# Kernel optimization log

Measured on AMD Instinct MI355X. Metric: run time of the kernel, lower is better.

## Reference

```python
import jax, jax.numpy as jnp
import numpy as np

B, S, E, H, R = 512, 50, 128, 8, 32
D = E // H  # depth per head
USERS, ITEMS, ALLSEQ, NCLASS = 50000, 20000, 20000, 5


def setup_inputs() -> dict:
    key = jax.random.key(0)
    ks = jax.random.split(key, 20)
    n = lambda k, shp, s=0.05: jax.random.normal(k, shp, dtype=jnp.float32) * s
    return {
        "user": jax.random.randint(ks[0], (B,), 0, USERS),
        "item": jax.random.randint(ks[1], (B,), 0, ITEMS),
        "neighbor": jax.random.randint(ks[2], (B, S), 0, USERS),
        "seq": jax.random.randint(ks[3], (B, S), 0, ALLSEQ),
        "user_emb_table": n(ks[4], (USERS, E)),
        "item_emb_table": n(ks[5], (ITEMS, E)),
        "user_item_LCU": n(ks[6], (ALLSEQ, R, E), 0.01),
        "item_user_LCU": n(ks[7], (ALLSEQ, R, E), 0.01),
        "wq": n(ks[8], (E, E)), "bq": jnp.zeros((E,), jnp.float32),
        "wk": n(ks[9], (E, E)), "bk": jnp.zeros((E,), jnp.float32),
        "wv": n(ks[10], (E, E)), "bv": jnp.zeros((E,), jnp.float32),
        "wo": n(ks[11], (E, E)), "bo": jnp.zeros((E,), jnp.float32),
        "fc_w": n(ks[12], (R, NCLASS)), "fc_b": jnp.zeros((NCLASS,), jnp.float32),
    }


def _forward(user, item, neighbor, seq,
             user_emb_table, item_emb_table, user_item_LCU, item_user_LCU,
             wq, bq, wk, bk, wv, bv, wo, bo, fc_w, fc_b):
    user_emb = user_emb_table[user]            # [B,E]
    neighbor_emb = user_emb_table[neighbor]    # [B,S,E]
    item_emb = item_emb_table[item]            # [B,E]
    weight = (neighbor > 0).astype(jnp.float32)  # [B,S] padding mask (1=real)

    # ---- single-query multi-head attention (use_attention=True) ----
    q = (user_emb @ wq + bq).reshape(B, H, D)                       # [B,H,D]
    k = (neighbor_emb @ wk + bk).reshape(B, S, H, D).transpose(0, 2, 1, 3)  # [B,H,S,D]
    v = (neighbor_emb @ wv + bv).reshape(B, S, H, D).transpose(0, 2, 1, 3)  # [B,H,S,D]
    logits = jnp.einsum('bhd,bhsd->bhs', q, k) / jnp.sqrt(jnp.float32(D))
    logits = logits + (1.0 - weight)[:, None, :] * (-1e9)           # mask padding
    attn = jax.nn.softmax(logits, axis=-1)                          # [B,H,S]
    ctx = attn[..., None] * v                                       # [B,H,S,D]
    ctx = ctx.transpose(0, 2, 1, 3).reshape(B, S, E)                # [B,S,E]
    neighbor_emb = ctx @ wo + bo                                    # [B,S,E]

    # ---- region embedding ----
    K_ui = user_item_LCU[seq]   # [B,S,R,E]
    K_iu = item_user_LCU[seq]   # [B,S,R,E]
    neighbor_profile = jnp.einsum('bsre,bse->bsr', K_iu, neighbor_emb)  # [B,S,R]
    item_profile = jnp.einsum('bsre,be->bsr', K_ui, item_emb)          # [B,S,R]
    neighbor_rating = neighbor_profile * item_profile * weight[:, :, None]
    user_rating_vector = jnp.max(neighbor_rating, axis=1)              # [B,R]

    # ---- rating classifier ----
    return jax.nn.softmax(user_rating_vector @ fc_w + fc_b, axis=-1)   # [B,NCLASS]


def reference(user, item, neighbor, seq,
              user_emb_table, item_emb_table, user_item_LCU, item_user_LCU,
              wq, bq, wk, bk, wv, bv, wo, bo, fc_w, fc_b):
    return _forward(user, item, neighbor, seq,
                    user_emb_table, item_emb_table, user_item_LCU, item_user_LCU,
                    wq, bq, wk, bk, wv, bv, wo, bo, fc_w, fc_b)
```

## Files before the change

### kernel.cpp

```cpp
#include <hip/hip_runtime.h>
#include <math.h>

#define BB 512
#define SS 50
#define EE 128
#define HH 8
#define RR 32
#define NC 5
#define NSEQ 20000
#define NBS (BB*SS)
#define LDK 136

typedef __attribute__((ext_vector_type(8))) __bf16 bf16x8;
typedef __attribute__((ext_vector_type(4))) float f32x4;
typedef __attribute__((ext_vector_type(4))) unsigned short us4;

__device__ __forceinline__ unsigned short f2bf(float f) {
    unsigned int u = __float_as_uint(f);
    unsigned int r = (u + 0x7fffu + ((u >> 16) & 1u)) >> 16;
    return (unsigned short)r;
}
__device__ __forceinline__ float bf2f(unsigned short s) {
    return __uint_as_float(((unsigned int)s) << 16);
}
__device__ __forceinline__ float dot4(const float4& a, const float4& b) {
    return a.x*b.x + a.y*b.y + a.z*b.z + a.w*b.w;
}

__global__ __launch_bounds__(128) void conv_kernel(const float* __restrict__ wv,
                                                   const float* __restrict__ wo,
                                                   unsigned short* __restrict__ wvT,
                                                   unsigned short* __restrict__ woT) {
    const int n = blockIdx.x & 127;
    const float* src = (blockIdx.x >> 7) ? wo : wv;
    unsigned short* dst = (blockIdx.x >> 7) ? woT : wvT;
    const int k = threadIdx.x;
    dst[n*EE + k] = f2bf(src[k*EE + n]);
}

__global__ __launch_bounds__(256) void hist_kernel(const int* __restrict__ seq,
                                                   int* __restrict__ hist) {
    int i = blockIdx.x * 256 + threadIdx.x;
    if (i < NBS) atomicAdd(&hist[seq[i]], 1);
}

__global__ __launch_bounds__(1024) void scan_kernel(int* __restrict__ hist,
                                                    int* __restrict__ hstart) {
    const int t = threadIdx.x;
    const int CH = 20;
    const int base = t * CH;
    int loc[CH];
    int s = 0;
    #pragma unroll
    for (int i = 0; i < CH; ++i) {
        int idx = base + i;
        int v = (idx < NSEQ) ? hist[idx] : 0;
        loc[i] = s; s += v;
    }
    const int lane = t & 63, w = t >> 6;
    int incl = s;
    #pragma unroll
    for (int off = 1; off < 64; off <<= 1) {
        int n = __shfl_up(incl, off);
        if (lane >= off) incl += n;
    }
    __shared__ int wsum[16];
    if (lane == 63) wsum[w] = incl;
    __syncthreads();
    if (t == 0) {
        int acc = 0;
        #pragma unroll
        for (int k = 0; k < 16; ++k) { int v = wsum[k]; wsum[k] = acc; acc += v; }
    }
    __syncthreads();
    const int excl = incl - s + wsum[w];
    #pragma unroll
    for (int i = 0; i < CH; ++i) {
        int idx = base + i;
        if (idx < NSEQ) {
            int e = excl + loc[i];
            hist[idx] = e;
            hstart[idx] = e;
        }
    }
    if (t == 0) hstart[NSEQ] = NBS;
}

__global__ __launch_bounds__(256) void scatter_kernel(const int* __restrict__ seq,
                                                      int* __restrict__ hist,
                                                      int* __restrict__ perm) {
    int i = blockIdx.x * 256 + threadIdx.x;
    if (i < NBS) {
        int pos = atomicAdd(&hist[seq[i]], 1);
        perm[pos] = i;
    }
}

__global__ __launch_bounds__(256, 4) void attn_kernel(
    const int* __restrict__ user,
    const int* __restrict__ neighbor,
    const float* __restrict__ uet,
    const float* __restrict__ wq, const float* __restrict__ bq,
    const float* __restrict__ wk, const float* __restrict__ bk,
    const float* __restrict__ bv, const float* __restrict__ bo,
    const unsigned short* __restrict__ wvT, const unsigned short* __restrict__ woT,
    float* __restrict__ ws_ne2)
{
    __shared__ unsigned short kA[64*LDK];
    __shared__ float ue[EE];
    __shared__ float qs[EE];
    __shared__ float qkv[EE][HH];
    __shared__ float qkb[HH];
    __shared__ float attn_s[HH][SS];
    __shared__ float maskadd[SS];

    const int b = blockIdx.x;
    const int t = threadIdx.x;

    if (t < EE) ue[t] = uet[(size_t)user[b]*EE + t];
    if (t < SS) maskadd[t] = (neighbor[b*SS + t] > 0) ? 0.f : -1e9f;
    for (int idx = t; idx < SS*32; idx += 256) {
        int s = idx >> 5, g = idx & 31;
        float4 v = ((const float4*)(uet + (size_t)neighbor[b*SS + s]*EE))[g];
        us4 o; o.x = f2bf(v.x); o.y = f2bf(v.y); o.z = f2bf(v.z); o.w = f2bf(v.w);
        *(us4*)&kA[s*LDK + g*4] = o;
    }
    for (int idx = t; idx < 14*LDK; idx += 256) {
        kA[50*LDK + idx] = 0;
    }
    __syncthreads();

    if (t < EE) {
        float acc = bq[t];
        #pragma unroll 4
        for (int e = 0; e < EE; ++e) acc = fmaf(ue[e], wq[e*EE + t], acc);
        qs[t] = acc;
    }
    __syncthreads();

    {
        const int e = t >> 1, h0 = (t & 1) * 4;
        const float* wrow = wk + e*EE;
        #pragma unroll
        for (int j = 0; j < 4; ++j) {
            int h = h0 + j;
            float acc = 0.f;
            #pragma unroll
            for (int d = 0; d < 16; ++d) acc = fmaf(qs[h*16 + d], wrow[h*16 + d], acc);
            qkv[e][h] = acc;
        }
    }
    if (t < HH) {
        float acc = 0.f;
        #pragma unroll
        for (int d = 0; d < 16; ++d) acc = fmaf(qs[t*16 + d], bk[t*16 + d], acc);
        qkb[t] = acc;
    }
    __syncthreads();

    if (t < HH*SS) {
        const int s = t >> 3, h = t & 7;
        float acc = 0.f;
        for (int e = 0; e < EE; ++e) {
            acc = fmaf(bf2f(kA[s*LDK + e]), qkv[e][h], acc);
        }
        attn_s[h][s] = (acc + qkb[h]) * 0.25f + maskadd[s];
    }
    __syncthreads();

    if (t < 64) {
        int h = t >> 3, l = t & 7;
        float mx = -3e38f;
        #pragma unroll
        for (int i = 0; i < 7; ++i) { int s = i*8 + l; if (s < SS) mx = fmaxf(mx, attn_s[h][s]); }
        mx = fmaxf(mx, __shfl_xor(mx, 1));
        mx = fmaxf(mx, __shfl_xor(mx, 2));
        mx = fmaxf(mx, __shfl_xor(mx, 4));
        float ev[7]; float sm_ = 0.f;
        #pragma unroll
        for (int i = 0; i < 7; ++i) {
            int s = i*8 + l; ev[i] = 0.f;
            if (s < SS) { ev[i] = expf(attn_s[h][s] - mx); sm_ += ev[i]; }
        }
        sm_ += __shfl_xor(sm_, 1);
        sm_ += __shfl_xor(sm_, 2);
        sm_ += __shfl_xor(sm_, 4);
        float inv = 1.f / sm_;
        #pragma unroll
        for (int i = 0; i < 7; ++i) { int s = i*8 + l; if (s < SS) attn_s[h][s] = ev[i] * inv; }
    }
    __syncthreads();

    const int w    = t >> 6;
    const int l    = t & 63;
    const int lrow = l & 15;
    const int kg   = l >> 4;

    bf16x8 a0 = *(const bf16x8*)&kA[(w*16 + lrow)*LDK +  0 + kg*8];
    bf16x8 a1 = *(const bf16x8*)&kA[(w*16 + lrow)*LDK + 32 + kg*8];
    bf16x8 a2 = *(const bf16x8*)&kA[(w*16 + lrow)*LDK + 64 + kg*8];
    bf16x8 a3 = *(const bf16x8*)&kA[(w*16 + lrow)*LDK + 96 + kg*8];

    f32x4 acc[8];
    #pragma unroll
    for (int nt = 0; nt < 8; ++nt) {
        const unsigned short* bp = wvT + (nt*16 + lrow)*EE + kg*8;
        bf16x8 b0 = *(const bf16x8*)&bp[0];
        bf16x8 b1 = *(const bf16x8*)&bp[32];
        bf16x8 b2 = *(const bf16x8*)&bp[64];
        bf16x8 b3 = *(const bf16x8*)&bp[96];
        f32x4 c = {0.f, 0.f, 0.f, 0.f};
        c = __builtin_amdgcn_mfma_f32_16x16x32_bf16(a0, b0, c, 0, 0, 0);
        c = __builtin_amdgcn_mfma_f32_16x16x32_bf16(a1, b1, c, 0, 0, 0);
        c = __builtin_amdgcn_mfma_f32_16x16x32_bf16(a2, b2, c, 0, 0, 0);
        c = __builtin_amdgcn_mfma_f32_16x16x32_bf16(a3, b3, c, 0, 0, 0);
        acc[nt] = c;
    }

    #pragma unroll
    for (int nt = 0; nt < 8; ++nt) {
        const int col = nt*16 + lrow;
        const float bvc = bv[col];
        #pragma unroll
        for (int rg = 0; rg < 4; ++rg) {
            const int row = w*16 + kg*4 + rg;
            const float av = (row < SS) ? attn_s[nt][row] : 0.f;
            kA[row*LDK + col] = f2bf((acc[nt][rg] + bvc) * av);
        }
    }
    __syncthreads();

    bf16x8 c0 = *(const bf16x8*)&kA[(w*16 + lrow)*LDK +  0 + kg*8];
    bf16x8 c1 = *(const bf16x8*)&kA[(w*16 + lrow)*LDK + 32 + kg*8];
    bf16x8 c2 = *(const bf16x8*)&kA[(w*16 + lrow)*LDK + 64 + kg*8];
    bf16x8 c3 = *(const bf16x8*)&kA[(w*16 + lrow)*LDK + 96 + kg*8];

    #pragma unroll
    for (int nt = 0; nt < 8; ++nt) {
        const unsigned short* bp = woT + (nt*16 + lrow)*EE + kg*8;
        bf16x8 b0 = *(const bf16x8*)&bp[0];
        bf16x8 b1 = *(const bf16x8*)&bp[32];
        bf16x8 b2 = *(const bf16x8*)&bp[64];
        bf16x8 b3 = *(const bf16x8*)&bp[96];
        f32x4 c = {0.f, 0.f, 0.f, 0.f};
        c = __builtin_amdgcn_mfma_f32_16x16x32_bf16(c0, b0, c, 0, 0, 0);
        c = __builtin_amdgcn_mfma_f32_16x16x32_bf16(c1, b1, c, 0, 0, 0);
        c = __builtin_amdgcn_mfma_f32_16x16x32_bf16(c2, b2, c, 0, 0, 0);
        c = __builtin_amdgcn_mfma_f32_16x16x32_bf16(c3, b3, c, 0, 0, 0);
        const int col = nt*16 + lrow;
        const float boc = bo[col];
        #pragma unroll
        for (int rg = 0; rg < 4; ++rg) {
            const int row = w*16 + kg*4 + rg;
            if (row < SS)
                ws_ne2[((size_t)b*SS + row)*EE + col] = c[rg] + boc;
        }
    }
}

__global__ __launch_bounds__(256, 6) void region_kernel(
    const int* __restrict__ neighbor, const int* __restrict__ item,
    const float* __restrict__ ui_lcu, const float* __restrict__ iu_lcu,
    const float* __restrict__ iet, const float* __restrict__ ws_ne2,
    const int* __restrict__ hstart, const int* __restrict__ perm,
    float* __restrict__ ws_rating)
{
    const int j = blockIdx.x;
    const int start = hstart[j];
    const int end   = hstart[j + 1];
    if (start >= end) return;

    const int t = threadIdx.x;
    const int r = t >> 3, l = t & 7;

    const float4* kiu_g = (const float4*)(iu_lcu + ((size_t)j*RR + r)*EE);
    const float4* kui_g = (const float4*)(ui_lcu + ((size_t)j*RR + r)*EE);
    float4 kiu_r[4], kui_r[4];
    #pragma unroll
    for (int i = 0; i < 4; ++i) {
        int c = l + 8*i;
        kiu_r[i] = kiu_g[c];
        kui_r[i] = kui_g[c];
    }

    __shared__ float ner[EE], ier[EE];
    const float4* n4 = (const float4*)ner;
    const float4* i4 = (const float4*)ier;

    for (int o = start; o < end; ++o) {
        const int bs = perm[o];
        const int b  = bs / SS;
        if (t < EE) ner[t] = ws_ne2[(size_t)bs*EE + t];
        else        ier[t - EE] = iet[(size_t)item[b]*EE + (t - EE)];
        __syncthreads();

        float np_ = 0.f, ip_ = 0.f;
        #pragma unroll
        for (int i = 0; i < 4; ++i) {
            int c = l + 8*i;
            np_ += dot4(kiu_r[i], n4[c]);
            ip_ += dot4(kui_r[i], i4[c]);
        }
        np_ += __shfl_xor(np_, 1); np_ += __shfl_xor(np_, 2); np_ += __shfl_xor(np_, 4);
        ip_ += __shfl_xor(ip_, 1); ip_ += __shfl_xor(ip_, 2); ip_ += __shfl_xor(ip_, 4);

        const float w = (neighbor[bs] > 0) ? 1.f : 0.f;
        if (l == 0) ws_rating[(size_t)bs*RR + r] = np_ * ip_ * w;
        if (o + 1 < end) __syncthreads();
    }
}

__global__ __launch_bounds__(256) void head_kernel(
    const float* __restrict__ ws_rating,
    const float* __restrict__ fc_w, const float* __restrict__ fc_b,
    float* __restrict__ out)
{
    __shared__ float part[8][RR];
    __shared__ float urv[RR];
    __shared__ float lg[NC];
    const int b = blockIdx.x, t = threadIdx.x;
    const int r = t & 31, sub = t >> 5;

    float m = -3e38f;
    for (int s = sub; s < SS; s += 8)
        m = fmaxf(m, ws_rating[((size_t)b*SS + s)*RR + r]);
    part[sub][r] = m;
    __syncthreads();
    if (t < RR) {
        float mm = part[0][t];
        #pragma unroll
        for (int k = 1; k < 8; ++k) mm = fmaxf(mm, part[k][t]);
        urv[t] = mm;
    }
    __syncthreads();
    if (t < NC) {
        float acc = fc_b[t];
        #pragma unroll
        for (int rr = 0; rr < RR; ++rr) acc = fmaf(urv[rr], fc_w[rr*NC + t], acc);
        lg[t] = acc;
    }
    __syncthreads();
    if (t < NC) {
        float mx = lg[0];
        #pragma unroll
        for (int c = 1; c < NC; ++c) mx = fmaxf(mx, lg[c]);
        float sm = 0.f;
        #pragma unroll
        for (int c = 0; c < NC; ++c) sm += expf(lg[c] - mx);
        out[b*NC + t] = expf(lg[t] - mx) / sm;
    }
}

extern "C" void kernel_launch(void* const* d_in, const int* in_sizes, int n_in,
                              void* d_out, int out_size, void* d_ws, size_t ws_size,
                              hipStream_t stream) {
    const int*   user     = (const int*)d_in[0];
    const int*   item     = (const int*)d_in[1];
    const int*   neighbor = (const int*)d_in[2];
    const int*   seq      = (const int*)d_in[3];
    const float* uet      = (const float*)d_in[4];
    const float* iet      = (const float*)d_in[5];
    const float* ui_lcu   = (const float*)d_in[6];
    const float* iu_lcu   = (const float*)d_in[7];
    const float* wq = (const float*)d_in[8];   const float* bq = (const float*)d_in[9];
    const float* wk = (const float*)d_in[10];  const float* bk = (const float*)d_in[11];
    const float* wv = (const float*)d_in[12];  const float* bv = (const float*)d_in[13];
    const float* wo = (const float*)d_in[14];  const float* bo = (const float*)d_in[15];
    const float* fcw = (const float*)d_in[16]; const float* fcb = (const float*)d_in[17];

    float* ws = (float*)d_ws;
    float* ws_ne2    = ws;
    float* ws_rating = ws_ne2 + (size_t)BB*SS*EE;
    unsigned short* wvT = (unsigned short*)(ws_rating + (size_t)BB*SS*RR);
    unsigned short* woT = wvT + EE*EE;
    int*   hist      = (int*)(woT + EE*EE);
    int*   hstart    = hist + NSEQ;
    int*   perm      = hstart + NSEQ + 1;
    float* out = (float*)d_out;

    hipLaunchKernelGGL(conv_kernel, dim3(256), dim3(128), 0, stream, wv, wo, wvT, woT);
    hipMemsetAsync(hist, 0, NSEQ * sizeof(int), stream);
    hipLaunchKernelGGL(hist_kernel, dim3((NBS + 255)/256), dim3(256), 0, stream, seq, hist);
    hipLaunchKernelGGL(scan_kernel, dim3(1), dim3(1024), 0, stream, hist, hstart);
    hipLaunchKernelGGL(scatter_kernel, dim3((NBS + 255)/256), dim3(256), 0, stream, seq, hist, perm);

    hipLaunchKernelGGL(attn_kernel, dim3(BB), dim3(256), 0, stream,
                       user, neighbor, uet,
                       wq, bq, wk, bk, bv, bo, wvT, woT, ws_ne2);

    hipLaunchKernelGGL(region_kernel, dim3(NSEQ), dim3(256), 0, stream,
                       neighbor, item, ui_lcu, iu_lcu, iet, ws_ne2, hstart, perm, ws_rating);

    hipLaunchKernelGGL(head_kernel, dim3(BB), dim3(256), 0, stream,
                       ws_rating, fcw, fcb, out);
}
```

Baseline: 182.9 us.

## Compute attention logits with MFMA and drop shared staging in region kernel

The attention kernel now stores the folded q·Wk vectors as a bf16 transposed tile and computes the 50×8 logits with 16x16x32 bf16 MFMA, reusing the neighbor A-fragments later for the V projection. This replaces a serial 128-step scalar FMA loop per thread. The region kernel now reads neighbor and item embeddings directly from global memory instead of staging them in shared memory, which removes two barriers per iteration, and it loads the LCU rows with nontemporal loads. The costs are bf16 rounding of the q·Wk product and redundant global reads across the 32 r-groups, which mostly hit cache.

```diff
diff --git a/kernel.cpp b/kernel.cpp
--- a/kernel.cpp
+++ b/kernel.cpp
@@ -20,11 +20,11 @@
     unsigned int r = (u + 0x7fffu + ((u >> 16) & 1u)) >> 16;
     return (unsigned short)r;
 }
-__device__ __forceinline__ float bf2f(unsigned short s) {
-    return __uint_as_float(((unsigned int)s) << 16);
-}
 __device__ __forceinline__ float dot4(const float4& a, const float4& b) {
     return a.x*b.x + a.y*b.y + a.z*b.z + a.w*b.w;
+}
+__device__ __forceinline__ float dot4v(const f32x4& a, const float4& b) {
+    return a[0]*b.x + a[1]*b.y + a[2]*b.z + a[3]*b.w;
 }
 
 __global__ __launch_bounds__(128) void conv_kernel(const float* __restrict__ wv,
@@ -107,27 +107,26 @@
     float* __restrict__ ws_ne2)
 {
     __shared__ unsigned short kA[64*LDK];
+    __shared__ unsigned short qkvT[16][EE];
     __shared__ float ue[EE];
     __shared__ float qs[EE];
-    __shared__ float qkv[EE][HH];
     __shared__ float qkb[HH];
-    __shared__ float attn_s[HH][SS];
-    __shared__ float maskadd[SS];
+    __shared__ float attn_s[HH][64];
+    __shared__ float maskadd[64];
 
     const int b = blockIdx.x;
     const int t = threadIdx.x;
 
     if (t < EE) ue[t] = uet[(size_t)user[b]*EE + t];
-    if (t < SS) maskadd[t] = (neighbor[b*SS + t] > 0) ? 0.f : -1e9f;
+    if (t < 64) maskadd[t] = (t < SS && neighbor[b*SS + t] > 0) ? 0.f : -1e9f;
     for (int idx = t; idx < SS*32; idx += 256) {
         int s = idx >> 5, g = idx & 31;
         float4 v = ((const float4*)(uet + (size_t)neighbor[b*SS + s]*EE))[g];
         us4 o; o.x = f2bf(v.x); o.y = f2bf(v.y); o.z = f2bf(v.z); o.w = f2bf(v.w);
         *(us4*)&kA[s*LDK + g*4] = o;
     }
-    for (int idx = t; idx < 14*LDK; idx += 256) {
-        kA[50*LDK + idx] = 0;
-    }
+    for (int idx = t; idx < 14*LDK; idx += 256) kA[50*LDK + idx] = 0;
+    for (int idx = t; idx < 8*EE; idx += 256) qkvT[8 + (idx >> 7)][idx & 127] = 0;
     __syncthreads();
 
     if (t < EE) {
@@ -147,7 +146,7 @@
             float acc = 0.f;
             #pragma unroll
             for (int d = 0; d < 16; ++d) acc = fmaf(qs[h*16 + d], wrow[h*16 + d], acc);
-            qkv[e][h] = acc;
+            qkvT[h][e] = f2bf(acc);
         }
     }
     if (t < HH) {
@@ -158,28 +157,49 @@
     }
     __syncthreads();
 
-    if (t < HH*SS) {
-        const int s = t >> 3, h = t & 7;
-        float acc = 0.f;
-        for (int e = 0; e < EE; ++e) {
-            acc = fmaf(bf2f(kA[s*LDK + e]), qkv[e][h], acc);
-        }
-        attn_s[h][s] = (acc + qkb[h]) * 0.25f + maskadd[s];
+    const int w    = t >> 6;
+    const int l    = t & 63;
+    const int lrow = l & 15;
+    const int kg   = l >> 4;
+
+    bf16x8 a0 = *(const bf16x8*)&kA[(w*16 + lrow)*LDK +  0 + kg*8];
+    bf16x8 a1 = *(const bf16x8*)&kA[(w*16 + lrow)*LDK + 32 + kg*8];
+    bf16x8 a2 = *(const bf16x8*)&kA[(w*16 + lrow)*LDK + 64 + kg*8];
+    bf16x8 a3 = *(const bf16x8*)&kA[(w*16 + lrow)*LDK + 96 + kg*8];
+
+    {
+        bf16x8 b0 = *(const bf16x8*)&qkvT[lrow][ 0 + kg*8];
+        bf16x8 b1 = *(const bf16x8*)&qkvT[lrow][32 + kg*8];
+        bf16x8 b2 = *(const bf16x8*)&qkvT[lrow][64 + kg*8];
+        bf16x8 b3 = *(const bf16x8*)&qkvT[lrow][96 + kg*8];
+        f32x4 c = {0.f, 0.f, 0.f, 0.f};
+        c = __builtin_amdgcn_mfma_f32_16x16x32_bf16(a0, b0, c, 0, 0, 0);
+        c = __builtin_amdgcn_mfma_f32_16x16x32_bf16(a1, b1, c, 0, 0, 0);
+        c = __builtin_amdgcn_mfma_f32_16x16x32_bf16(a2, b2, c, 0, 0, 0);
+        c = __builtin_amdgcn_mfma_f32_16x16x32_bf16(a3, b3, c, 0, 0, 0);
+        const int h = lrow;
+        if (h < HH) {
+            #pragma unroll
+            for (int rg = 0; rg < 4; ++rg) {
+                const int row = w*16 + kg*4 + rg;
+                attn_s[h][row] = (c[rg] + qkb[h]) * 0.25f + maskadd[row];
+            }
+        }
     }
     __syncthreads();
 
     if (t < 64) {
-        int h = t >> 3, l = t & 7;
+        int h = t >> 3, ll = t & 7;
         float mx = -3e38f;
         #pragma unroll
-        for (int i = 0; i < 7; ++i) { int s = i*8 + l; if (s < SS) mx = fmaxf(mx, attn_s[h][s]); }
+        for (int i = 0; i < 7; ++i) { int s = i*8 + ll; if (s < SS) mx = fmaxf(mx, attn_s[h][s]); }
         mx = fmaxf(mx, __shfl_xor(mx, 1));
         mx = fmaxf(mx, __shfl_xor(mx, 2));
         mx = fmaxf(mx, __shfl_xor(mx, 4));
         float ev[7]; float sm_ = 0.f;
         #pragma unroll
         for (int i = 0; i < 7; ++i) {
-            int s = i*8 + l; ev[i] = 0.f;
+            int s = i*8 + ll; ev[i] = 0.f;
             if (s < SS) { ev[i] = expf(attn_s[h][s] - mx); sm_ += ev[i]; }
         }
         sm_ += __shfl_xor(sm_, 1);
@@ -187,19 +207,9 @@
         sm_ += __shfl_xor(sm_, 4);
         float inv = 1.f / sm_;
         #pragma unroll
-        for (int i = 0; i < 7; ++i) { int s = i*8 + l; if (s < SS) attn_s[h][s] = ev[i] * inv; }
-    }
-    __syncthreads();
-
-    const int w    = t >> 6;
-    const int l    = t & 63;
-    const int lrow = l & 15;
-    const int kg   = l >> 4;
-
-    bf16x8 a0 = *(const bf16x8*)&kA[(w*16 + lrow)*LDK +  0 + kg*8];
-    bf16x8 a1 = *(const bf16x8*)&kA[(w*16 + lrow)*LDK + 32 + kg*8];
-    bf16x8 a2 = *(const bf16x8*)&kA[(w*16 + lrow)*LDK + 64 + kg*8];
-    bf16x8 a3 = *(const bf16x8*)&kA[(w*16 + lrow)*LDK + 96 + kg*8];
+        for (int i = 0; i < 7; ++i) { int s = i*8 + ll; if (s < SS) attn_s[h][s] = ev[i] * inv; }
+    }
+    __syncthreads();
 
     f32x4 acc[8];
     #pragma unroll
@@ -216,7 +226,6 @@
         c = __builtin_amdgcn_mfma_f32_16x16x32_bf16(a3, b3, c, 0, 0, 0);
         acc[nt] = c;
     }
-
     #pragma unroll
     for (int nt = 0; nt < 8; ++nt) {
         const int col = nt*16 + lrow;
@@ -273,40 +282,33 @@
     const int t = threadIdx.x;
     const int r = t >> 3, l = t & 7;
 
-    const float4* kiu_g = (const float4*)(iu_lcu + ((size_t)j*RR + r)*EE);
-    const float4* kui_g = (const float4*)(ui_lcu + ((size_t)j*RR + r)*EE);
-    float4 kiu_r[4], kui_r[4];
+    const f32x4* kiu_g = (const f32x4*)(iu_lcu + ((size_t)j*RR + r)*EE);
+    const f32x4* kui_g = (const f32x4*)(ui_lcu + ((size_t)j*RR + r)*EE);
+    f32x4 kiu_r[4], kui_r[4];
     #pragma unroll
     for (int i = 0; i < 4; ++i) {
-        int c = l + 8*i;
-        kiu_r[i] = kiu_g[c];
-        kui_r[i] = kui_g[c];
-    }
-
-    __shared__ float ner[EE], ier[EE];
-    const float4* n4 = (const float4*)ner;
-    const float4* i4 = (const float4*)ier;
+        kiu_r[i] = __builtin_nontemporal_load(&kiu_g[l + 8*i]);
+        kui_r[i] = __builtin_nontemporal_load(&kui_g[l + 8*i]);
+    }
 
     for (int o = start; o < end; ++o) {
         const int bs = perm[o];
         const int b  = bs / SS;
-        if (t < EE) ner[t] = ws_ne2[(size_t)bs*EE + t];
-        else        ier[t - EE] = iet[(size_t)item[b]*EE + (t - EE)];
-        __syncthreads();
+        const float4* n4 = (const float4*)(ws_ne2 + (size_t)bs*EE);
+        const float4* i4 = (const float4*)(iet + (size_t)item[b]*EE);
 
         float np_ = 0.f, ip_ = 0.f;
         #pragma unroll
         for (int i = 0; i < 4; ++i) {
             int c = l + 8*i;
-            np_ += dot4(kiu_r[i], n4[c]);
-            ip_ += dot4(kui_r[i], i4[c]);
+            np_ += dot4v(kiu_r[i], n4[c]);
+            ip_ += dot4v(kui_r[i], i4[c]);
         }
         np_ += __shfl_xor(np_, 1); np_ += __shfl_xor(np_, 2); np_ += __shfl_xor(np_, 4);
         ip_ += __shfl_xor(ip_, 1); ip_ += __shfl_xor(ip_, 2); ip_ += __shfl_xor(ip_, 4);
 
         const float w = (neighbor[bs] > 0) ? 1.f : 0.f;
         if (l == 0) ws_rating[(size_t)bs*RR + r] = np_ * ip_ * w;
-        if (o + 1 < end) __syncthreads();
     }
 }
 
```

Result: faster. 175.6 us (-4.0%).
